# Performance work log

Measured on AMD Instinct MI355X. Metric: run time of the kernel, lower is better.

Reference implementation:

```python
import jax, jax.numpy as jnp
import numpy as np

D = 20       # bond_dim (= virtual_dim = per-module output_dim)
BATCH = 128
BN_EPS = 1e-5


def _unfold(t, h, w, n):
    # torch x.unfold(2,h,h).unfold(3,w,w).reshape(b, C, -1, n)
    B, C, H, W = t.shape
    t = t.reshape(B, C, H // h, h, W // w, w).transpose(0, 1, 2, 4, 3, 5)
    return t.reshape(B, C, -1, n)


def _mps(x, cores, label):
    # x: [b, C, P, n] site values; cores: [P, n, D, F, D] with F = 2*C; label: [P, D, O, D]
    feat = jnp.concatenate([x, 1.0 - x], axis=1)              # [b, F, P, n]  ([x, 1-x] feature map)
    M = jnp.einsum('bfpn,pnufv->npbuv', feat, cores)           # [n, P, b, D, D] site matrices
    v = jnp.full((cores.shape[2],), cores.shape[2] ** -0.5, dtype=x.dtype)  # boundary vector
    left = jnp.einsum('u,pbuv->pbv', v, M[0])
    for i in range(1, M.shape[0]):                             # n is small & static (4 or 16)
        left = jnp.einsum('pbu,pbuv->pbv', left, M[i])
    return jnp.einsum('pbu,puov,v->bpo', left, label, v)       # [b, P, O]


def _bn(y, gamma, beta):
    # training-mode BatchNorm1d over channel axis 1 of [b, C, L]
    mean = y.mean(axis=(0, 2), keepdims=True)
    var = y.var(axis=(0, 2), keepdims=True)
    return (y - mean) * jax.lax.rsqrt(var + BN_EPS) * gamma[None, :, None] + beta[None, :, None]


def setup_inputs() -> dict:
    key = jax.random.key(0)
    ks = jax.random.split(key, 9)
    f32 = jnp.float32
    def core(k, shape):
        F = shape[-2]
        return (jax.random.normal(k, shape, f32) * np.float32(np.sqrt(3.0 / (D * F))))
    def lab(k, shape):
        return jax.random.normal(k, shape, f32) * np.float32(D ** -0.5)
    x = jax.random.uniform(ks[0], (BATCH, 48, 32, 32), f32)
    return {
        'x': x,
        'cores1': core(ks[1], (256, 4, D, 96, D)), 'label1': lab(ks[2], (256, D, D, D)),
        'g1': jnp.ones(256, f32), 'b1': jnp.zeros(256, f32),
        'cores2': core(ks[3], (64, 4, D, 2 * D, D)), 'label2': lab(ks[4], (64, D, D, D)),
        'g2': jnp.ones(64, f32), 'b2': jnp.zeros(64, f32),
        'cores3': core(ks[5], (16, 4, D, 2 * D, D)), 'label3': lab(ks[6], (16, D, D, D)),
        'g3': jnp.ones(16, f32), 'b3': jnp.zeros(16, f32),
        'coresF': core(ks[7], (16, D, 2 * D, D)), 'labelF': lab(ks[8], (D, 10, D)),
    }


def reference(x, cores1, label1, g1, b1, cores2, label2, g2, b2,
              cores3, label3, g3, b3, coresF, labelF):
    b = x.shape[0]
    # stage 1: 256 patch-experts over 4 sites each
    x1 = _unfold(x, 16, 16, 4)                  # [b, 48, 256, 4]
    y = _mps(x1, cores1, label1)                # [b, 256, D]
    y = _bn(y, g1, b1).reshape(b, D, 16, 16)    # faithful patch<->bond mixing view
    # stage 2: 64 experts
    y2 = _unfold(y, 8, 8, 4)                    # [b, D, 64, 4]
    y = _mps(y2, cores2, label2)                # [b, 64, D]
    y = _bn(y, g2, b2).reshape(b, D, 8, 8)
    # stage 3: 16 experts
    y3 = _unfold(y, 4, 4, 4)                    # [b, D, 16, 4]
    y = _mps(y3, cores3, label3)                # [b, 16, D]
    y = _bn(y, g3, b3)
    # final MPS over the 16 expert outputs (channels = D)
    y = y.transpose(0, 2, 1)[:, :, None, :]     # [b, D, 1, 16]
    out = _mps(y, coresF[None], labelF[None])   # [b, 1, 10]
    return out[:, 0, :]                         # squeeze -> [b, 10]
```

## Files before the change

### kernel.cpp

```cpp
#include <hip/hip_runtime.h>

#define VB 0.22360679774997896f

typedef __attribute__((ext_vector_type(8))) _Float16 half8;
typedef __attribute__((ext_vector_type(4))) float f32x4;

#define Z1_OFF   0
#define Z2_OFF   655360
#define Z3_OFF   819200
#define GS1_OFF  860160
#define GQ1_OFF  860416
#define GS2_OFF  860672
#define GQ2_OFF  860736
#define GS3_OFF  860800
#define GQ3_OFF  860816
#define LV2_OFF  963232
#define LV3_OFF  988832
#define WH2_OFF  995232
#define WH3_OFF  4272032

#define WAVEBAR() __builtin_amdgcn_wave_barrier()

#define BARRIER_LGKM()                                        \
    asm volatile("s_waitcnt lgkmcnt(0)" ::: "memory");        \
    __builtin_amdgcn_sched_barrier(0);                        \
    __builtin_amdgcn_s_barrier();

#define LOADW(W, ci)                                                          \
    {                                                                         \
        const float* wp_ = wbase + (size_t)(ci) * 7680;                       \
        _Pragma("unroll")                                                     \
        for (int k = 0; k < 4; ++k) {                                         \
            int i4 = tid + k * 512;                                           \
            if (i4 < 1920) W[k] = *(const float4*)(wp_ + i4 * 4);             \
        }                                                                     \
    }

#define SCATW(W, DST)                                                         \
    {                                                                         \
        _Pragma("unroll")                                                     \
        for (int k = 0; k < 4; ++k) {                                         \
            int i4 = tid + k * 512;                                           \
            if (i4 < 1920) {                                                  \
                float vals[4] = {W[k].x, W[k].y, W[k].z, W[k].w};             \
                _Pragma("unroll")                                             \
                for (int t = 0; t < 4; ++t)                                   \
                    DST[sAddr[k][t]] = (_Float16)vals[t];                     \
            }                                                                 \
        }                                                                     \
    }

#define CHUNKD(ci, W)                                                         \
    {                                                                         \
        f32x4 acc[5];                                                         \
        _Pragma("unroll")                                                     \
        for (int nt = 0; nt < 5; ++nt) acc[nt] = (f32x4){0.f, 0.f, 0.f, 0.f};\
        _Pragma("unroll")                                                     \
        for (int ks = 0; ks < 3; ++ks) {                                      \
            _Pragma("unroll")                                                 \
            for (int nt = 0; nt < 5; ++nt) {                                  \
                half8 bf = *(const half8*)&Fcur[((ks * 5 + nt) * 64 + l) * 8];\
                acc[nt] = __builtin_amdgcn_mfma_f32_16x16x32_f16(             \
                    af[ks], bf, acc[nt], 0, 0, 0);                            \
            }                                                                 \
        }                                                                     \
        _Pragma("unroll")                                                     \
        for (int nt = 0; nt < 5; ++nt) {                                      \
            _Pragma("unroll")                                                 \
            for (int r = 0; r < 4; ++r)                                       \
                Mw[(hi * 4 + r) * 84 + nt * 16 + row16] = acc[nt][r];         \
        }                                                                     \
        WAVEBAR();                                                            \
        _Pragma("unroll")                                                     \
        for (int ul = 0; ul < 4; ++ul) {                                      \
            float lvx = lw[bQ * 20 + ((ci) % 5) * 4 + ul];                    \
            _Pragma("unroll")                                                 \
            for (int j = 0; j < 5; ++j)                                       \
                lacc[j] += lvx * Mw[bQ * 84 + ul * 20 + mh * 5 + j];          \
        }                                                                     \
        WAVEBAR();                                                            \
        BARRIER_LGKM();                                                       \
        if ((ci) < 19) { SCATW(W, Fnxt) }                                     \
        BARRIER_LGKM();                                                       \
        { _Float16* t_ = Fcur; Fcur = Fnxt; Fnxt = t_; }                      \
        if ((ci) <= 16) { LOADW(W, (ci) + 3) }                                \
    }

#define SITE(nv, W0, W1, W2, W3, W4)                                          \
    {                                                                         \
        _Pragma("unroll")                                                     \
        for (int k = 0; k < 12; ++k) {                                        \
            int idx = l + k * 64;                                             \
            float v = ((nv) == 0) ? xr[k].x : ((nv) == 1) ? xr[k].y           \
                    : ((nv) == 2) ? xr[k].z : xr[k].w;                        \
            xSw[idx] = v;                                                     \
        }                                                                     \
        WAVEBAR();                                                            \
        half8 af[3];                                                          \
        _Pragma("unroll")                                                     \
        for (int ks = 0; ks < 3; ++ks) {                                      \
            int f0 = ks * 32 + hi * 8;                                        \
            int cc = (f0 < 48) ? f0 : f0 - 48;                                \
            float4 a  = *(const float4*)&xSw[row16 * 48 + cc];                \
            float4 b2 = *(const float4*)&xSw[row16 * 48 + cc + 4];            \
            float vv[8] = {a.x, a.y, a.z, a.w, b2.x, b2.y, b2.z, b2.w};       \
            bool inv = (f0 >= 48);                                            \
            half8 hv;                                                         \
            _Pragma("unroll")                                                 \
            for (int j = 0; j < 8; ++j)                                       \
                hv[j] = (_Float16)(inv ? (1.f - vv[j]) : vv[j]);              \
            af[ks] = hv;                                                      \
        }                                                                     \
        WAVEBAR();                                                            \
        CHUNKD((nv) * 5 + 0, W0)                                              \
        CHUNKD((nv) * 5 + 1, W1)                                              \
        CHUNKD((nv) * 5 + 2, W2)                                              \
        CHUNKD((nv) * 5 + 3, W3)                                              \
        CHUNKD((nv) * 5 + 4, W4)                                              \
        _Pragma("unroll")                                                     \
        for (int j = 0; j < 5; ++j) {                                         \
            lw[bQ * 20 + mh * 5 + j] = lacc[j]; lacc[j] = 0.f;                \
        }                                                                     \
        WAVEBAR();                                                            \
    }

__global__ __launch_bounds__(512, 2)
void fused1_kernel(const float* __restrict__ x, const float* __restrict__ cores1,
                   const float* __restrict__ label1,
                   const float* __restrict__ cores2, const float* __restrict__ cores3,
                   const float* __restrict__ label2, const float* __restrict__ label3,
                   float* __restrict__ z1, float* __restrict__ gs, float* __restrict__ gq,
                   _Float16* __restrict__ Wh2, _Float16* __restrict__ Wh3,
                   float* __restrict__ lv2, float* __restrict__ lv3,
                   float* __restrict__ gzero)
{
    __shared__ __align__(16) float xS[8 * 768];
    __shared__ __align__(16) _Float16 Fbuf[2][7680];
    __shared__ __align__(16) float MchunkS[8 * 16 * 84];
    __shared__ __align__(16) float leftS[8 * 320];
    __shared__ __align__(16) float labvS[400];
    __shared__ float redS[16];

    const int tid = threadIdx.x;
    const int bid = blockIdx.x;
    const int p   = (bid & 7) * 32 + (bid >> 3);
    const int wv  = tid >> 6, l = tid & 63;
    float* xSw = xS + wv * 768;
    float* Mw  = MchunkS + wv * 1344;
    float* lw  = leftS + wv * 320;
    const int row16 = l & 15, hi = l >> 4;
    const int bQ = l >> 2,   mh = l & 3;
    const int hh  = (p >> 7) * 16 + ((p >> 2) & 15);
    const int ww0 = ((p >> 6) & 1) * 16 + (p & 3) * 4;

    float4 xr[12];
    #pragma unroll
    for (int k = 0; k < 12; ++k) {
        int idx = l + k * 64;
        int br = idx / 48, c = idx - br * 48;
        xr[k] = *(const float4*)(x + (((size_t)((wv * 16 + br) * 48 + c)) << 10)
                                   + hh * 32 + ww0);
    }

    int sAddr[4][4];
    #pragma unroll
    for (int k = 0; k < 4; ++k) {
        int i4 = tid + k * 512;
        if (i4 < 1920) {
            #pragma unroll
            for (int t = 0; t < 4; ++t) {
                int e = i4 * 4 + t;
                int v = e % 20;
                int r = e / 20;
                int f = r % 96;
                int ul = r / 96;
                int c = ul * 20 + v;
                sAddr[k][t] = (((f >> 5) * 5 + (c >> 4)) * 64 +
                               ((f >> 3) & 3) * 16 + (c & 15)) * 8 + (f & 7);
            }
        }
    }

    #pragma unroll
    for (int j = 0; j < 5; ++j) lw[bQ * 20 + mh * 5 + j] = VB;
    WAVEBAR();

    float lacc[5] = {0.f, 0.f, 0.f, 0.f, 0.f};
    float4 wrA[4], wrB[4];
    const float* wbase = cores1 + (size_t)p * 153600;

    _Float16* Fcur = &Fbuf[0][0];
    _Float16* Fnxt = &Fbuf[1][0];

    LOADW(wrA, 0)
    SCATW(wrA, Fcur)
    LOADW(wrA, 1)
    LOADW(wrB, 2)
    BARRIER_LGKM();

    if (tid < 400) {
        const float* lb = label1 + (size_t)p * 8000 + tid * 20;
        float s = 0.f;
        #pragma unroll
        for (int vv = 0; vv < 20; ++vv) s += lb[vv];
        labvS[tid] = s * VB;
    }

    SITE(0, wrA, wrB, wrA, wrB, wrA)
    SITE(1, wrB, wrA, wrB, wrA, wrB)
    SITE(2, wrA, wrB, wrA, wrB, wrA)
    SITE(3, wrB, wrA, wrB, wrA, wrB)

    float yv[5] = {0.f, 0.f, 0.f, 0.f, 0.f};
    #pragma unroll
    for (int u = 0; u < 20; ++u) {
        float lu = lw[bQ * 20 + u];
        #pragma unroll
        for (int j = 0; j < 5; ++j) yv[j] += lu * labvS[u * 20 + mh * 5 + j];
    }
    float s = 0.f, s2 = 0.f;
    #pragma unroll
    for (int j = 0; j < 5; ++j) {
        z1[(size_t)(wv * 16 + bQ) * 5120 + p * 20 + mh * 5 + j] = yv[j];
        s += yv[j]; s2 += yv[j] * yv[j];
    }
    #pragma unroll
    for (int off = 32; off > 0; off >>= 1) {
        s  += __shfl_down(s, off);
        s2 += __shfl_down(s2, off);
    }
    if (l == 0) { redS[wv] = s; redS[8 + wv] = s2; }
    __syncthreads();
    if (tid == 0) {
        float S = 0.f, Q = 0.f;
        #pragma unroll
        for (int w2 = 0; w2 < 8; ++w2) { S += redS[w2]; Q += redS[8 + w2]; }
        gs[p] = S; gq[p] = Q;
    }

    __syncthreads();
    _Float16* fragS = (_Float16*)xS;

    #pragma unroll
    for (int k = 0; k < 2; ++k) {
        int i = tid + k * 512;
        if (i < 640) ((uint4*)fragS)[i] = (uint4){0, 0, 0, 0};
    }
    __syncthreads();

    for (int slab = bid; slab < 1600; slab += 256) {
        const float* src;
        _Float16* dst;
        if (slab < 1280) { src = cores2 + (size_t)slab * 3200;          dst = Wh2 + (size_t)slab * 5120; }
        else             { src = cores3 + (size_t)(slab - 1280) * 3200; dst = Wh3 + (size_t)(slab - 1280) * 5120; }
        #pragma unroll
        for (int k = 0; k < 2; ++k) {
            int i4 = tid + k * 512;
            if (i4 < 800) {
                float4 w = *(const float4*)(src + i4 * 4);
                float vals[4] = {w.x, w.y, w.z, w.w};
                #pragma unroll
                for (int t = 0; t < 4; ++t) {
                    int e = i4 * 4 + t;
                    int v = e % 20;
                    int r = e / 20;
                    int f = r % 40;
                    int ul = r / 40;
                    int c = ul * 20 + v;
                    int addr = (((f >> 5) * 5 + (c >> 4)) * 64 +
                                ((f >> 3) & 3) * 16 + (c & 15)) * 8 + (f & 7);
                    fragS[addr] = (_Float16)vals[t];
                }
            }
        }
        __syncthreads();
        #pragma unroll
        for (int k = 0; k < 2; ++k) {
            int i = tid + k * 512;
            if (i < 640) ((uint4*)dst)[i] = ((const uint4*)fragS)[i];
        }
        __syncthreads();
    }

    if (bid < 80) {
        const float* lb;
        float* ov;
        if (bid < 64) { lb = label2 + (size_t)bid * 8000;        ov = lv2 + bid * 400; }
        else          { lb = label3 + (size_t)(bid - 64) * 8000; ov = lv3 + (bid - 64) * 400; }
        if (tid < 400) {
            const float4* sp = (const float4*)(lb + tid * 20);
            float acc = 0.f;
            #pragma unroll
            for (int t = 0; t < 5; ++t) {
                float4 w = sp[t];
                acc += w.x + w.y + w.z + w.w;
            }
            ov[tid] = acc * VB;
        }
    }
    if (bid == 255 && tid < 160) gzero[tid] = 0.f;
}

#define UCBODYN(ucv, CUR, NXT)                                                   \
    {                                                                            \
        if ((ucv) < 4) {                                                         \
            const _Float16* bptr = whp + (size_t)((ucv) + 1) * 5120;             \
            _Pragma("unroll")                                                    \
            for (int q = 0; q < 10; ++q)                                         \
                NXT[q] = *(const half8*)(bptr + (q * 64 + l) * 8);               \
        }                                                                        \
        f32x4 acc[5];                                                            \
        _Pragma("unroll")                                                        \
        for (int nt = 0; nt < 5; ++nt) acc[nt] = (f32x4){0.f, 0.f, 0.f, 0.f};    \
        _Pragma("unroll")                                                        \
        for (int ks = 0; ks < 2; ++ks) {                                         \
            _Pragma("unroll")                                                    \
            for (int nt = 0; nt < 5; ++nt)                                       \
                acc[nt] = __builtin_amdgcn_mfma_f32_16x16x32_f16(                \
                    af[ks], CUR[ks * 5 + nt], acc[nt], 0, 0, 0);                 \
        }                                                                        \
        _Pragma("unroll")                                                        \
        for (int nt = 0; nt < 5; ++nt) {                                         \
            _Pragma("unroll")                                                    \
            for (int r = 0; r < 4; ++r)                                          \
                Mw[(hi * 4 + r) * 84 + nt * 16 + row16] = acc[nt][r];            \
        }                                                                        \
        WAVEBAR();                                                               \
        _Pragma("unroll")                                                        \
        for (int ul = 0; ul < 4; ++ul) {                                         \
            float lvx = lw[bQ * 20 + (ucv) * 4 + ul];                            \
            _Pragma("unroll")                                                    \
            for (int j = 0; j < 5; ++j)                                          \
                lacc[j] += lvx * Mw[bQ * 84 + ul * 20 + mh * 5 + j];             \
        }                                                                        \
        WAVEBAR();                                                               \
    }

template <int STAGE>
__global__ __launch_bounds__(256, 2)
void stageN_kernel(const float* __restrict__ zin, const _Float16* __restrict__ Wh,
                   const float* __restrict__ labv,
                   const float* __restrict__ gsin, const float* __restrict__ gqin,
                   const float* __restrict__ gam,  const float* __restrict__ bet,
                   float* __restrict__ zout,
                   float* __restrict__ gsout, float* __restrict__ gqout)
{
    constexpr int ZIN  = (STAGE == 2) ? 5120 : 1280;
    constexpr int ZOUT = (STAGE == 2) ? 1280 : 320;
    constexpr int JUMP = (STAGE == 2) ? 256 : 64;

    __shared__ __align__(16) float zS[4 * 320];
    __shared__ float scS[4 * 20], shS[4 * 20];
    __shared__ __align__(16) float MchunkS[4 * 16 * 84];
    __shared__ __align__(16) float leftS[4 * 320];

    const int tid = threadIdx.x;
    const int p   = blockIdx.x;
    const int bh  = blockIdx.y;
    const int wv  = tid >> 6, l = tid & 63;
    float* zSw = zS + wv * 320;
    float* scw = scS + wv * 20;
    float* shw = shS + wv * 20;
    float* Mw  = MchunkS + wv * 1344;
    float* lw  = leftS + wv * 320;
    const int row16 = l & 15, hi = l >> 4;
    const int bQ = l >> 2,   mh = l & 3;
    const int bg = bh * 64;

    #pragma unroll
    for (int j = 0; j < 5; ++j) lw[bQ * 20 + mh * 5 + j] = VB;
    WAVEBAR();

    float lacc[5] = {0.f, 0.f, 0.f, 0.f, 0.f};

    #pragma unroll 1
    for (int n = 0; n < 4; ++n) {
        int hh, ww;
        if (STAGE == 2) { hh = (p >> 5) * 8 + ((p >> 1) & 7); ww = ((p >> 4) & 1) * 8 + (p & 1) * 4 + n; }
        else            { hh = (p >> 3) * 4 + (p & 3);        ww = ((p >> 2) & 1) * 4 + n; }
        const int oo = (STAGE == 2) ? (hh * 16 + ww) : (hh * 8 + ww);

        if (l < 20) {
            int ch = (l * JUMP + oo) / 20;
            float mean = gsin[ch] * (1.f / 2560.f);
            float var  = gqin[ch] * (1.f / 2560.f) - mean * mean;
            float rstd = rsqrtf(var + 1e-5f);
            float sc = gam[ch] * rstd;
            scw[l] = sc;
            shw[l] = bet[ch] - mean * sc;
        }
        WAVEBAR();
        #pragma unroll
        for (int q = 0; q < 5; ++q) {
            int d = hi * 5 + q;
            float zraw = zin[(size_t)(bg + wv * 16 + row16) * ZIN + d * JUMP + oo];
            zSw[row16 * 20 + d] = zraw * scw[d] + shw[d];
        }
        WAVEBAR();
        half8 af[2];
        #pragma unroll
        for (int ks = 0; ks < 2; ++ks) {
            int f0 = ks * 32 + hi * 8;
            half8 hv;
            #pragma unroll
            for (int j = 0; j < 8; ++j) {
                int f = f0 + j;
                float val;
                if (f < 20)      val = zSw[row16 * 20 + f];
                else if (f < 40) val = 1.f - zSw[row16 * 20 + f - 20];
                else             val = 0.f;
                hv[j] = (_Float16)val;
            }
            af[ks] = hv;
        }
        WAVEBAR();

        const _Float16* whp = Wh + (size_t)((p * 4 + n) * 5) * 5120;
        half8 bA[10], bB[10];
        {
            #pragma unroll
            for (int q = 0; q < 10; ++q) bA[q] = *(const half8*)(whp + (q * 64 + l) * 8);
        }
        UCBODYN(0, bA, bB)
        UCBODYN(1, bB, bA)
        UCBODYN(2, bA, bB)
        UCBODYN(3, bB, bA)
        UCBODYN(4, bA, bB)

        #pragma unroll
        for (int j = 0; j < 5; ++j) { lw[bQ * 20 + mh * 5 + j] = lacc[j]; lacc[j] = 0.f; }
        WAVEBAR();
    }

    const float* lvp = labv + p * 400;
    #pragma unroll
    for (int k = 0; k < 7; ++k) { int i = l + k * 64; if (i < 400) Mw[i] = lvp[i]; }
    WAVEBAR();
    float yv[5] = {0.f, 0.f, 0.f, 0.f, 0.f};
    #pragma unroll
    for (int u = 0; u < 20; ++u) {
        float lu = lw[bQ * 20 + u];
        #pragma unroll
        for (int j = 0; j < 5; ++j) yv[j] += lu * Mw[u * 20 + mh * 5 + j];
    }
    float s = 0.f, s2 = 0.f;
    #pragma unroll
    for (int j = 0; j < 5; ++j) {
        zout[(size_t)(bg + wv * 16 + bQ) * ZOUT + p * 20 + mh * 5 + j] = yv[j];
        s += yv[j]; s2 += yv[j] * yv[j];
    }
    #pragma unroll
    for (int off = 32; off > 0; off >>= 1) {
        s  += __shfl_down(s, off);
        s2 += __shfl_down(s2, off);
    }
    if ((tid & 63) == 0) {
        atomicAdd(&gsout[p], s);
        atomicAdd(&gqout[p], s2);
    }
}

__global__ __launch_bounds__(256, 4)
void final_kernel(const float* __restrict__ z3,
                  const float* __restrict__ coresF,
                  const float* __restrict__ labelF,
                  const float* __restrict__ g3,
                  const float* __restrict__ b3,
                  const float* __restrict__ gsum3,
                  const float* __restrict__ gsq3,
                  float* __restrict__ out)
{
    __shared__ __align__(16) float fS[16 * 40];
    __shared__ __align__(16) float MS[16 * 400];
    __shared__ float lvS[200];
    __shared__ float scS[16], shS[16];
    __shared__ float leftS[20];

    const int b   = blockIdx.x;
    const int tid = threadIdx.x;

    if (tid < 16) {
        float mean = gsum3[tid] * (1.f / 2560.f);
        float var  = gsq3[tid] * (1.f / 2560.f) - mean * mean;
        float rstd = rsqrtf(var + 1e-5f);
        float sc   = g3[tid] * rstd;
        scS[tid] = sc;
        shS[tid] = b3[tid] - mean * sc;
    }
    __syncthreads();

    for (int i = tid; i < 640; i += 256) {
        int n = i / 40, f = i - n * 40;
        float raw = z3[(size_t)b * 320 + n * 20 + (f % 20)];
        float val = raw * scS[n] + shS[n];
        fS[i] = (f < 20) ? val : (1.f - val);
    }
    for (int i = tid; i < 200; i += 256) {
        int u = i / 10, o = i - u * 10;
        const float* lb = labelF + (size_t)(u * 10 + o) * 20;
        float s = 0.f;
        #pragma unroll
        for (int vv = 0; vv < 20; ++vv) s += lb[vv];
        lvS[i] = s * VB;
    }
    __syncthreads();

    for (int i = tid; i < 6400; i += 256) {
        int n = i / 400, uv = i - n * 400;
        int u = uv / 20, v = uv - u * 20;
        const float* wb = coresF + ((size_t)(n * 20 + u) * 40) * 20 + v;
        const float* fb = fS + n * 40;
        float acc = 0.f;
        #pragma unroll
        for (int f = 0; f < 40; ++f) acc += fb[f] * wb[f * 20];
        MS[i] = acc;
    }
    __syncthreads();

    if (tid < 64) {
        if (tid < 20) leftS[tid] = VB;
        WAVEBAR();
        #pragma unroll 1
        for (int n = 0; n < 16; ++n) {
            float tmp = 0.f;
            if (tid < 20) {
                #pragma unroll
                for (int u = 0; u < 20; ++u) tmp += leftS[u] * MS[n * 400 + u * 20 + tid];
            }
            WAVEBAR();
            if (tid < 20) leftS[tid] = tmp;
            WAVEBAR();
        }
        if (tid < 10) {
            float s = 0.f;
            #pragma unroll
            for (int u = 0; u < 20; ++u) s += leftS[u] * lvS[u * 10 + tid];
            out[b * 10 + tid] = s;
        }
    }
}

extern "C" void kernel_launch(void* const* d_in, const int* in_sizes, int n_in,
                              void* d_out, int out_size, void* d_ws, size_t ws_size,
                              hipStream_t stream)
{
    const float* x      = (const float*)d_in[0];
    const float* cores1 = (const float*)d_in[1];
    const float* label1 = (const float*)d_in[2];
    const float* g1     = (const float*)d_in[3];
    const float* b1     = (const float*)d_in[4];
    const float* cores2 = (const float*)d_in[5];
    const float* label2 = (const float*)d_in[6];
    const float* g2     = (const float*)d_in[7];
    const float* b2     = (const float*)d_in[8];
    const float* cores3 = (const float*)d_in[9];
    const float* label3 = (const float*)d_in[10];
    const float* g3     = (const float*)d_in[11];
    const float* b3     = (const float*)d_in[12];
    const float* coresF = (const float*)d_in[13];
    const float* labelF = (const float*)d_in[14];

    float* ws  = (float*)d_ws;
    float* z1  = ws + Z1_OFF;
    float* z2  = ws + Z2_OFF;
    float* z3  = ws + Z3_OFF;
    float* gs1 = ws + GS1_OFF; float* gq1 = ws + GQ1_OFF;
    float* gs2 = ws + GS2_OFF; float* gq2 = ws + GQ2_OFF;
    float* gs3 = ws + GS3_OFF; float* gq3 = ws + GQ3_OFF;
    float* lv2 = ws + LV2_OFF;
    float* lv3 = ws + LV3_OFF;
    _Float16* Wh2 = (_Float16*)(ws + WH2_OFF);
    _Float16* Wh3 = (_Float16*)(ws + WH3_OFF);

    fused1_kernel<<<256, 512, 0, stream>>>(x, cores1, label1,
                                           cores2, cores3, label2, label3,
                                           z1, gs1, gq1,
                                           Wh2, Wh3, lv2, lv3, gs2);
    stageN_kernel<2><<<dim3(64, 2), 256, 0, stream>>>(z1, Wh2, lv2, gs1, gq1, g1, b1,
                                                      z2, gs2, gq2);
    stageN_kernel<3><<<dim3(16, 2), 256, 0, stream>>>(z2, Wh3, lv3, gs2, gq2, g2, b2,
                                                      z3, gs3, gq3);
    final_kernel<<<128, 256, 0, stream>>>(z3, coresF, labelF, g3, b3,
                                          gs3, gq3, (float*)d_out);
}
```

Before: 107.5 us.

## Split stage-1 blocks across batch halves with atomic BN statistic accumulation

```diff
diff --git a/kernel.cpp b/kernel.cpp
--- a/kernel.cpp
+++ b/kernel.cpp
@@ -30,8 +30,8 @@
     {                                                                         \
         const float* wp_ = wbase + (size_t)(ci) * 7680;                       \
         _Pragma("unroll")                                                     \
-        for (int k = 0; k < 4; ++k) {                                         \
-            int i4 = tid + k * 512;                                           \
+        for (int k = 0; k < 8; ++k) {                                         \
+            int i4 = tid + k * 256;                                           \
             if (i4 < 1920) W[k] = *(const float4*)(wp_ + i4 * 4);             \
         }                                                                     \
     }
@@ -39,8 +39,8 @@
 #define SCATW(W, DST)                                                         \
     {                                                                         \
         _Pragma("unroll")                                                     \
-        for (int k = 0; k < 4; ++k) {                                         \
-            int i4 = tid + k * 512;                                           \
+        for (int k = 0; k < 8; ++k) {                                         \
+            int i4 = tid + k * 256;                                           \
             if (i4 < 1920) {                                                  \
                 float vals[4] = {W[k].x, W[k].y, W[k].z, W[k].w};             \
                 _Pragma("unroll")                                             \
@@ -124,7 +124,7 @@
         WAVEBAR();                                                            \
     }
 
-__global__ __launch_bounds__(512, 2)
+__global__ __launch_bounds__(256, 2)
 void fused1_kernel(const float* __restrict__ x, const float* __restrict__ cores1,
                    const float* __restrict__ label1,
                    const float* __restrict__ cores2, const float* __restrict__ cores3,
@@ -134,22 +134,24 @@
                    float* __restrict__ lv2, float* __restrict__ lv3,
                    float* __restrict__ gzero)
 {
-    __shared__ __align__(16) float xS[8 * 768];
+    __shared__ __align__(16) float xS[4 * 768];
     __shared__ __align__(16) _Float16 Fbuf[2][7680];
-    __shared__ __align__(16) float MchunkS[8 * 16 * 84];
-    __shared__ __align__(16) float leftS[8 * 320];
+    __shared__ __align__(16) float MchunkS[4 * 16 * 84];
+    __shared__ __align__(16) float leftS[4 * 320];
     __shared__ __align__(16) float labvS[400];
-    __shared__ float redS[16];
-
-    const int tid = threadIdx.x;
-    const int bid = blockIdx.x;
-    const int p   = (bid & 7) * 32 + (bid >> 3);
-    const int wv  = tid >> 6, l = tid & 63;
+
+    const int tid  = threadIdx.x;
+    const int bid  = blockIdx.x;
+    const int orig = bid & 255;
+    const int bh   = bid >> 8;
+    const int p    = (orig & 7) * 32 + (orig >> 3);
+    const int wv   = tid >> 6, l = tid & 63;
     float* xSw = xS + wv * 768;
     float* Mw  = MchunkS + wv * 1344;
     float* lw  = leftS + wv * 320;
     const int row16 = l & 15, hi = l >> 4;
     const int bQ = l >> 2,   mh = l & 3;
+    const int bg = bh * 64;
     const int hh  = (p >> 7) * 16 + ((p >> 2) & 15);
     const int ww0 = ((p >> 6) & 1) * 16 + (p & 3) * 4;
 
@@ -158,14 +160,14 @@
     for (int k = 0; k < 12; ++k) {
         int idx = l + k * 64;
         int br = idx / 48, c = idx - br * 48;
-        xr[k] = *(const float4*)(x + (((size_t)((wv * 16 + br) * 48 + c)) << 10)
+        xr[k] = *(const float4*)(x + (((size_t)((bg + wv * 16 + br) * 48 + c)) << 10)
                                    + hh * 32 + ww0);
     }
 
-    int sAddr[4][4];
-    #pragma unroll
-    for (int k = 0; k < 4; ++k) {
-        int i4 = tid + k * 512;
+    int sAddr[8][4];
+    #pragma unroll
+    for (int k = 0; k < 8; ++k) {
+        int i4 = tid + k * 256;
         if (i4 < 1920) {
             #pragma unroll
             for (int t = 0; t < 4; ++t) {
@@ -186,7 +188,7 @@
     WAVEBAR();
 
     float lacc[5] = {0.f, 0.f, 0.f, 0.f, 0.f};
-    float4 wrA[4], wrB[4];
+    float4 wrA[8], wrB[8];
     const float* wbase = cores1 + (size_t)p * 153600;
 
     _Float16* Fcur = &Fbuf[0][0];
@@ -198,12 +200,12 @@
     LOADW(wrB, 2)
     BARRIER_LGKM();
 
-    if (tid < 400) {
-        const float* lb = label1 + (size_t)p * 8000 + tid * 20;
+    for (int i = tid; i < 400; i += 256) {
+        const float* lb = label1 + (size_t)p * 8000 + i * 20;
         float s = 0.f;
         #pragma unroll
         for (int vv = 0; vv < 20; ++vv) s += lb[vv];
-        labvS[tid] = s * VB;
+        labvS[i] = s * VB;
     }
 
     SITE(0, wrA, wrB, wrA, wrB, wrA)
@@ -221,7 +223,7 @@
     float s = 0.f, s2 = 0.f;
     #pragma unroll
     for (int j = 0; j < 5; ++j) {
-        z1[(size_t)(wv * 16 + bQ) * 5120 + p * 20 + mh * 5 + j] = yv[j];
+        z1[(size_t)(bg + wv * 16 + bQ) * 5120 + p * 20 + mh * 5 + j] = yv[j];
         s += yv[j]; s2 += yv[j] * yv[j];
     }
     #pragma unroll
@@ -229,33 +231,26 @@
         s  += __shfl_down(s, off);
         s2 += __shfl_down(s2, off);
     }
-    if (l == 0) { redS[wv] = s; redS[8 + wv] = s2; }
-    __syncthreads();
-    if (tid == 0) {
-        float S = 0.f, Q = 0.f;
-        #pragma unroll
-        for (int w2 = 0; w2 < 8; ++w2) { S += redS[w2]; Q += redS[8 + w2]; }
-        gs[p] = S; gq[p] = Q;
-    }
+    if (l == 0) { atomicAdd(&gs[p], s); atomicAdd(&gq[p], s2); }
 
     __syncthreads();
     _Float16* fragS = (_Float16*)xS;
 
     #pragma unroll
-    for (int k = 0; k < 2; ++k) {
-        int i = tid + k * 512;
+    for (int k = 0; k < 3; ++k) {
+        int i = tid + k * 256;
         if (i < 640) ((uint4*)fragS)[i] = (uint4){0, 0, 0, 0};
     }
     __syncthreads();
 
-    for (int slab = bid; slab < 1600; slab += 256) {
+    for (int slab = bid; slab < 1600; slab += 512) {
         const float* src;
         _Float16* dst;
         if (slab < 1280) { src = cores2 + (size_t)slab * 3200;          dst = Wh2 + (size_t)slab * 5120; }
         else             { src = cores3 + (size_t)(slab - 1280) * 3200; dst = Wh3 + (size_t)(slab - 1280) * 5120; }
         #pragma unroll
-        for (int k = 0; k < 2; ++k) {
-            int i4 = tid + k * 512;
+        for (int k = 0; k < 4; ++k) {
+            int i4 = tid + k * 256;
             if (i4 < 800) {
                 float4 w = *(const float4*)(src + i4 * 4);
                 float vals[4] = {w.x, w.y, w.z, w.w};
@@ -275,8 +270,8 @@
         }
         __syncthreads();
         #pragma unroll
-        for (int k = 0; k < 2; ++k) {
-            int i = tid + k * 512;
+        for (int k = 0; k < 3; ++k) {
+            int i = tid + k * 256;
             if (i < 640) ((uint4*)dst)[i] = ((const uint4*)fragS)[i];
         }
         __syncthreads();
@@ -287,18 +282,18 @@
         float* ov;
         if (bid < 64) { lb = label2 + (size_t)bid * 8000;        ov = lv2 + bid * 400; }
         else          { lb = label3 + (size_t)(bid - 64) * 8000; ov = lv3 + (bid - 64) * 400; }
-        if (tid < 400) {
-            const float4* sp = (const float4*)(lb + tid * 20);
+        for (int i = tid; i < 400; i += 256) {
+            const float4* sp = (const float4*)(lb + i * 20);
             float acc = 0.f;
             #pragma unroll
             for (int t = 0; t < 5; ++t) {
                 float4 w = sp[t];
                 acc += w.x + w.y + w.z + w.w;
             }
-            ov[tid] = acc * VB;
-        }
-    }
-    if (bid == 255 && tid < 160) gzero[tid] = 0.f;
+            ov[i] = acc * VB;
+        }
+    }
+    if (bid == 511 && tid < 160) gzero[tid] = 0.f;
 }
 
 #define UCBODYN(ucv, CUR, NXT)                                                   \
@@ -572,7 +567,9 @@
     _Float16* Wh2 = (_Float16*)(ws + WH2_OFF);
     _Float16* Wh3 = (_Float16*)(ws + WH3_OFF);
 
-    fused1_kernel<<<256, 512, 0, stream>>>(x, cores1, label1,
+    hipMemsetAsync(gs1, 0, 512 * sizeof(float), stream);
+
+    fused1_kernel<<<512, 256, 0, stream>>>(x, cores1, label1,
                                            cores2, cores3, label2, label3,
                                            z1, gs1, gq1,
                                            Wh2, Wh3, lv2, lv3, gs2);
```

Result: slower. 194.9 us (+81.3%).
